# Performance work log

Hardware: AMD Instinct MI355X
Metric: run time of the kernel (lower is better)

Reference implementation:

```python
import jax, jax.numpy as jnp
import numpy as np

K_CLUSTERS = 64   # hardcoded k=64 in get_kmenas_prototypes
KM_ITERS = 10     # KMeans(max_iter=10)


def _kmeans_one_hot(x):
    """x: (B, N, C) points. Returns one-hot cluster masks (B, K, N)."""
    B, N, C = x.shape
    init_idx = jnp.round(jnp.linspace(0, N - 1, K_CLUSTERS)).astype(jnp.int32)

    def per_item(pts):  # (N, C)
        p2 = (pts * pts).sum(-1)  # (N,)

        def assign(cent):
            c2 = (cent * cent).sum(-1)
            d = p2[:, None] + c2[None, :] - 2.0 * (pts @ cent.T)  # (N, K)
            return jnp.argmin(d, axis=1)

        def step(i, cent):
            lab = assign(cent)
            oh = jax.nn.one_hot(lab, K_CLUSTERS, dtype=pts.dtype)  # (N, K)
            cnt = oh.sum(0)
            sums = oh.T @ pts  # (K, C)
            return jnp.where(cnt[:, None] > 0, sums / jnp.maximum(cnt, 1.0)[:, None], cent)

        cent = jax.lax.fori_loop(0, KM_ITERS, step, pts[init_idx])
        lab = assign(cent)
        return jax.nn.one_hot(lab, K_CLUSTERS, dtype=pts.dtype).T  # (K, N)

    return jax.vmap(per_item)(x)


def reference(target, ref, sqz_w, sqz_b, slot_w, slot_b, Wq, Wk, Wv, Wo):
    B, Cin, H, W = target.shape
    Cout = sqz_w.shape[0]
    R = ref.shape[0]
    HW = H * W

    # 1x1 convs
    sqz_target = jnp.einsum('bchw,oc->bohw', target, sqz_w) + sqz_b[None, :, None, None]
    slot_target = jnp.einsum('bchw,oc->bohw', target, slot_w) + slot_b[None, :, None, None]

    xt = sqz_target.reshape(B, Cout, HW)  # (B, C, HW)

    # KMeans prototypes (clustering mask is detached in the original)
    mask = jax.lax.stop_gradient(_kmeans_one_hot(xt.transpose(0, 2, 1)))  # (B, K, HW)
    target_pt = jnp.einsum('bkn,bcn->bkc', mask, xt)  # (B, K, C)

    # slot prototypes: softmax over slot/channel dim (dim=1)
    ss = jax.nn.softmax(slot_target.reshape(B, -1, HW), axis=1)  # (B, S, HW)
    slot_pt = jnp.einsum('bsn,bcn->bsc', ss, xt)  # (B, S, C)
    slot_mask = ss.reshape(B, -1, H, W)

    # ref prototypes: mask = feature itself, softmax over spatial dim (dim=2)
    sqz_ref = jnp.einsum('rbchw,oc->rbohw', ref, sqz_w) + sqz_b[None, None, :, None, None]
    xr = sqz_ref.reshape(R, B, Cout, HW)
    ssr = jax.nn.softmax(xr, axis=3)
    ref_pt = jnp.einsum('rbcn,rbdn->rbcd', ssr, xr)  # (R, B, C, C)

    # Feature_Aggregation_Transformer: cross-attention, queries = kmeans tokens,
    # kv = flattened ref prototype tokens (b, R*C, C)
    kv = ref_pt.transpose(1, 0, 2, 3).reshape(B, R * Cout, Cout)
    q = target_pt @ Wq
    k = kv @ Wk
    v = kv @ Wv
    scale = 1.0 / jnp.sqrt(jnp.asarray(Cout, q.dtype))
    attn = jax.nn.softmax(jnp.einsum('bqc,bkc->bqk', q, k) * scale, axis=-1)
    agg_pt = jnp.einsum('bqk,bkc->bqc', attn, v) @ Wo + target_pt  # (B, K, C)

    return (sqz_target, agg_pt, ref_pt, slot_pt, slot_mask)


def setup_inputs() -> dict:
    key = jax.random.key(0)
    ks = jax.random.split(key, 12)
    B, Cin, Cout, S, H, W, R = 8, 512, 128, 16, 64, 64, 3
    w = lambda k, shp: (jax.random.normal(k, shp, dtype=jnp.float32) * 0.02)
    return {
        'target': jax.random.normal(ks[0], (B, Cin, H, W), dtype=jnp.float32),
        'ref': jax.random.normal(ks[1], (R, B, Cin, H, W), dtype=jnp.float32),
        'sqz_w': w(ks[2], (Cout, Cin)),
        'sqz_b': jnp.zeros((Cout,), dtype=jnp.float32),
        'slot_w': w(ks[3], (S, Cin)),
        'slot_b': jnp.zeros((S,), dtype=jnp.float32),
        'Wq': w(ks[4], (Cout, Cout)),
        'Wk': w(ks[5], (Cout, Cout)),
        'Wv': w(ks[6], (Cout, Cout)),
        'Wo': w(ks[7], (Cout, Cout)),
    }
```

## Files before the change

kernel.cpp:

```cpp
#include <hip/hip_runtime.h>

#define NB 8
#define CIN 512
#define CO 128
#define NS 16
#define NHW 4096
#define NR 3
#define NK 64
#define KMITERS 10

typedef __attribute__((ext_vector_type(8))) short s16x8;
typedef __attribute__((ext_vector_type(4))) float f32x4;

static __device__ __forceinline__ void bsplit(float x, short& h, short& l) {
    union { float f; unsigned u; } a; a.f = x;
    h = (short)(a.u >> 16);
    union { unsigned u; float f; } hf; hf.u = a.u & 0xFFFF0000u;
    union { float f; unsigned u; } r; r.f = x - hf.f;
    l = (short)(r.u >> 16);
}

__global__ __launch_bounds__(256) void conv_mfma(const float* __restrict__ X,
    const float* __restrict__ Wt, const float* __restrict__ bias, float* __restrict__ out)
{
    __shared__ short sWh[128 * 40];
    __shared__ short sWl[128 * 40];
    __shared__ float sX[32 * 133];
    const int g = blockIdx.y;
    const int n0 = blockIdx.x * 128;
    const int tid = threadIdx.x;
    const int lane = tid & 63, w = tid >> 6;
    const int l15 = lane & 15, quad = lane >> 4;
    const int wm = (w & 1) * 64, wn = (w >> 1) * 64;

    f32x4 acc[4][4];
#pragma unroll
    for (int i = 0; i < 4; ++i)
#pragma unroll
        for (int j = 0; j < 4; ++j) acc[i][j] = (f32x4){0.f, 0.f, 0.f, 0.f};

    for (int c0 = 0; c0 < CIN; c0 += 32) {
        if (c0) __syncthreads();
#pragma unroll
        for (int r = 0; r < 4; ++r) {
            int e = r * 1024 + tid * 4;
            int m = e >> 5, cc = e & 31;
            const float4 wv = *(const float4*)&Wt[(size_t)m * CIN + c0 + cc];
            short h0, l0, h1, l1, h2, l2, h3, l3;
            bsplit(wv.x, h0, l0); bsplit(wv.y, h1, l1);
            bsplit(wv.z, h2, l2); bsplit(wv.w, h3, l3);
            *(short4*)&sWh[m * 40 + cc] = make_short4(h0, h1, h2, h3);
            *(short4*)&sWl[m * 40 + cc] = make_short4(l0, l1, l2, l3);
        }
#pragma unroll
        for (int r = 0; r < 4; ++r) {
            int e = r * 1024 + tid * 4;
            int k = e >> 7, n = e & 127;
            const float4 xv = *(const float4*)&X[((size_t)g * CIN + c0 + k) * NHW + n0 + n];
            float* p = &sX[k * 133 + n];
            p[0] = xv.x; p[1] = xv.y; p[2] = xv.z; p[3] = xv.w;
        }
        __syncthreads();

        s16x8 ah[4], al[4];
#pragma unroll
        for (int mt = 0; mt < 4; ++mt) {
            int m = wm + mt * 16 + l15;
            ah[mt] = *(const s16x8*)&sWh[m * 40 + quad * 8];
            al[mt] = *(const s16x8*)&sWl[m * 40 + quad * 8];
        }
#pragma unroll
        for (int nt = 0; nt < 4; ++nt) {
            int n = wn + nt * 16 + l15;
            s16x8 bh, bl;
#pragma unroll
            for (int jj = 0; jj < 8; ++jj) {
                float xv = sX[(quad * 8 + jj) * 133 + n];
                short h, l; bsplit(xv, h, l);
                bh[jj] = h; bl[jj] = l;
            }
#pragma unroll
            for (int mt = 0; mt < 4; ++mt) {
                acc[mt][nt] = __builtin_amdgcn_mfma_f32_16x16x32_bf16(ah[mt], bh, acc[mt][nt], 0, 0, 0);
                acc[mt][nt] = __builtin_amdgcn_mfma_f32_16x16x32_bf16(ah[mt], bl, acc[mt][nt], 0, 0, 0);
                acc[mt][nt] = __builtin_amdgcn_mfma_f32_16x16x32_bf16(al[mt], bh, acc[mt][nt], 0, 0, 0);
            }
        }
    }
#pragma unroll
    for (int mt = 0; mt < 4; ++mt) {
#pragma unroll
        for (int reg = 0; reg < 4; ++reg) {
            int m = wm + mt * 16 + quad * 4 + reg;
            float bv = bias[m];
#pragma unroll
            for (int nt = 0; nt < 4; ++nt) {
                int n = wn + nt * 16 + l15;
                out[((size_t)g * CO + m) * NHW + n0 + n] = acc[mt][nt][reg] + bv;
            }
        }
    }
}

template<int BM, int BN, int BK, int TM, int TN>
__global__ __launch_bounds__(256) void conv1x1(const float* __restrict__ X,
    const float* __restrict__ Wt, const float* __restrict__ bias,
    float* __restrict__ outf)
{
    __shared__ float sW[BK][BM + 1];
    __shared__ float sX2[BK][BN + 1];
    const int g  = blockIdx.z;
    const int m0 = blockIdx.y * BM;
    const int n0 = blockIdx.x * BN;
    const int tid = threadIdx.x;
    const int tn = tid % (BN / TN);
    const int tm = tid / (BN / TN);
    const int O = gridDim.y * BM;

    float acc[TM][TN];
#pragma unroll
    for (int i = 0; i < TM; ++i)
#pragma unroll
        for (int j = 0; j < TN; ++j) acc[i][j] = 0.f;

    for (int c0 = 0; c0 < CIN; c0 += BK) {
#pragma unroll
        for (int idx = tid; idx < BM * BK; idx += 256) {
            int k = idx % BK, i = idx / BK;
            sW[k][i] = Wt[(size_t)(m0 + i) * CIN + c0 + k];
        }
#pragma unroll
        for (int idx = tid; idx < BK * BN; idx += 256) {
            int j = idx % BN, k = idx / BN;
            sX2[k][j] = X[((size_t)g * CIN + c0 + k) * NHW + n0 + j];
        }
        __syncthreads();
#pragma unroll
        for (int k = 0; k < BK; ++k) {
            float a[TM], bb[TN];
#pragma unroll
            for (int i = 0; i < TM; ++i) a[i] = sW[k][tm * TM + i];
#pragma unroll
            for (int j = 0; j < TN; ++j) bb[j] = sX2[k][tn * TN + j];
#pragma unroll
            for (int i = 0; i < TM; ++i)
#pragma unroll
                for (int j = 0; j < TN; ++j) acc[i][j] = fmaf(a[i], bb[j], acc[i][j]);
        }
        __syncthreads();
    }
#pragma unroll
    for (int i = 0; i < TM; ++i) {
        int m = m0 + tm * TM + i;
        float bv = bias[m];
#pragma unroll
        for (int j = 0; j < TN; ++j) {
            int n = n0 + tn * TN + j;
            outf[((size_t)g * O + m) * NHW + n] = acc[i][j] + bv;
        }
    }
}

__global__ void km_init(const float* __restrict__ xt, float* __restrict__ cent) {
    int idx = blockIdx.x * 256 + threadIdx.x;
    if (idx >= NB * NK * CO) return;
    int c = idx % CO;
    int k = (idx / CO) % NK;
    int b = idx / (CO * NK);
    cent[idx] = xt[((size_t)b * CO + c) * NHW + 65 * k];
}

__global__ __launch_bounds__(256) void km_label(const float* __restrict__ xt,
    const float* __restrict__ cent, float* __restrict__ psums, float* __restrict__ pcnt)
{
    __shared__ float sCent[64 * 129];
    __shared__ float sXs[32 * 133];
    __shared__ float sC2[64];
    __shared__ float sCnt[64];
    __shared__ int sLab[128];
    const int b = blockIdx.y, nb = blockIdx.x;
    const int n0 = nb * 128;
    const int tid = threadIdx.x;

#pragma unroll
    for (int r = 0; r < 8; ++r) {
        int e = r * 1024 + tid * 4;
        int k = e >> 7, c = e & 127;
        const float4 cv = *(const float4*)&cent[((size_t)b * NK + k) * CO + c];
        float* p = &sCent[k * 129 + c];
        p[0] = cv.x; p[1] = cv.y; p[2] = cv.z; p[3] = cv.w;
    }
    __syncthreads();
    if (tid < 64) {
        float s = 0.f;
        for (int c = 0; c < CO; ++c) { float v = sCent[tid * 129 + c]; s = fmaf(v, v, s); }
        sC2[tid] = s;
    }

    const int tn = tid & 7, tm = tid >> 3;
    float dot[4][8];
    float p2[4];
#pragma unroll
    for (int i = 0; i < 4; ++i) {
        p2[i] = 0.f;
#pragma unroll
        for (int j = 0; j < 8; ++j) dot[i][j] = 0.f;
    }
    for (int cc = 0; cc < 4; ++cc) {
        __syncthreads();
#pragma unroll
        for (int r = 0; r < 4; ++r) {
            int e = r * 1024 + tid * 4;
            int c = e >> 7, n = e & 127;
            const float4 xv = *(const float4*)&xt[((size_t)b * CO + cc * 32 + c) * NHW + n0 + n];
            float* p = &sXs[c * 133 + n];
            p[0] = xv.x; p[1] = xv.y; p[2] = xv.z; p[3] = xv.w;
        }
        __syncthreads();
        for (int c4 = 0; c4 < 8; ++c4) {
            float xv[4][4];
#pragma unroll
            for (int j = 0; j < 4; ++j)
#pragma unroll
                for (int i = 0; i < 4; ++i)
                    xv[j][i] = sXs[(c4 * 4 + j) * 133 + tm * 4 + i];
#pragma unroll
            for (int j = 0; j < 4; ++j)
#pragma unroll
                for (int i = 0; i < 4; ++i)
                    p2[i] = fmaf(xv[j][i], xv[j][i], p2[i]);
#pragma unroll
            for (int jj = 0; jj < 8; ++jj) {
                int k = tn * 8 + jj;
#pragma unroll
                for (int j = 0; j < 4; ++j) {
                    float cv = sCent[k * 129 + cc * 32 + c4 * 4 + j];
#pragma unroll
                    for (int i = 0; i < 4; ++i)
                        dot[i][jj] = fmaf(xv[j][i], cv, dot[i][jj]);
                }
            }
        }
    }
#pragma unroll
    for (int i = 0; i < 4; ++i) {
        int lab = tn * 8;
        float bd = p2[i] + sC2[tn * 8] - 2.f * dot[i][0];
#pragma unroll
        for (int jj = 1; jj < 8; ++jj) {
            int k = tn * 8 + jj;
            float d = p2[i] + sC2[k] - 2.f * dot[i][jj];
            if (d < bd) { bd = d; lab = k; }
        }
#pragma unroll
        for (int off = 1; off < 8; off <<= 1) {
            float d2 = __shfl_xor(bd, off);
            int l2 = __shfl_xor(lab, off);
            if (d2 < bd || (d2 == bd && l2 < lab)) { bd = d2; lab = l2; }
        }
        if (tn == 0) sLab[tm * 4 + i] = lab;
    }
    __syncthreads();
    for (int e = tid; e < 64 * 129; e += 256) sCent[e] = 0.f;
    if (tid < 64) sCnt[tid] = 0.f;
    __syncthreads();
    if (tid < 128) atomicAdd(&sCnt[sLab[tid]], 1.f);
    const int cq = tid & 31, sh = tid >> 5;
    for (int cc = 0; cc < 4; ++cc) {
        __syncthreads();
#pragma unroll
        for (int r = 0; r < 4; ++r) {
            int e = r * 1024 + tid * 4;
            int c = e >> 7, n = e & 127;
            const float4 xv = *(const float4*)&xt[((size_t)b * CO + cc * 32 + c) * NHW + n0 + n];
            float* p = &sXs[c * 133 + n];
            p[0] = xv.x; p[1] = xv.y; p[2] = xv.z; p[3] = xv.w;
        }
        __syncthreads();
        int c = cc * 32 + cq;
        for (int ii = 0; ii < 16; ++ii) {
            int p = sh * 16 + ii;
            atomicAdd(&sCent[sLab[p] * 129 + c], sXs[cq * 133 + p]);
        }
    }
    __syncthreads();
    float* ps = &psums[((size_t)b * 32 + nb) * (NK * CO)];
    for (int e = tid; e < NK * CO; e += 256) {
        int k = e >> 7, c = e & 127;
        ps[e] = sCent[k * 129 + c];
    }
    if (tid < 64) pcnt[((size_t)b * 32 + nb) * 64 + tid] = sCnt[tid];
}

__global__ void km_update2(float* __restrict__ cent, float* __restrict__ tpt,
    const float* __restrict__ psums, const float* __restrict__ pcnt, int mode)
{
    const int k = blockIdx.x, b = blockIdx.y, c = threadIdx.x;
    float s = 0.f;
    for (int nb = 0; nb < 32; ++nb)
        s += psums[((size_t)b * 32 + nb) * (NK * CO) + k * CO + c];
    if (mode) { tpt[((size_t)b * NK + k) * CO + c] = s; return; }
    float cn = 0.f;
    for (int nb = 0; nb < 32; ++nb)
        cn += pcnt[((size_t)b * 32 + nb) * 64 + k];
    if (cn > 0.f) cent[((size_t)b * NK + k) * CO + c] = s / fmaxf(cn, 1.f);
}

__global__ void slot_softmax(const float* __restrict__ ssb, float* __restrict__ out4) {
    int idx = blockIdx.x * 256 + threadIdx.x;
    if (idx >= NB * NHW) return;
    int b = idx / NHW, n = idx % NHW;
    float v[NS];
    float m = -1e30f;
#pragma unroll
    for (int s = 0; s < NS; ++s) { v[s] = ssb[((size_t)b * NS + s) * NHW + n]; m = fmaxf(m, v[s]); }
    float sum = 0.f;
#pragma unroll
    for (int s = 0; s < NS; ++s) { v[s] = expf(v[s] - m); sum += v[s]; }
    float inv = 1.f / sum;
#pragma unroll
    for (int s = 0; s < NS; ++s)
        out4[((size_t)b * NS + s) * NHW + n] = v[s] * inv;
}

__global__ __launch_bounds__(256) void slot_pt_kernel(const float* __restrict__ ss,
    const float* __restrict__ xt, float* __restrict__ spt)
{
    __shared__ float sS[NS][257];
    __shared__ float sX2[32][257];
    const int b = blockIdx.y;
    const int n0 = blockIdx.x * 256;
    const int tid = threadIdx.x;
    for (int i = tid; i < NS * 256; i += 256) {
        int s = i >> 8, nn = i & 255;
        sS[s][nn] = ss[((size_t)b * NS + s) * NHW + n0 + nn];
    }
    const int c = tid & 31;
    const int sA = tid >> 5;
    for (int cg = 0; cg < 4; ++cg) {
        __syncthreads();
        for (int i = tid; i < 32 * 256; i += 256) {
            int cc = i >> 8, nn = i & 255;
            sX2[cc][nn] = xt[((size_t)b * CO + cg * 32 + cc) * NHW + n0 + nn];
        }
        __syncthreads();
        float a0 = 0.f, a1 = 0.f;
        for (int nn = 0; nn < 256; ++nn) {
            float x = sX2[c][nn];
            a0 = fmaf(x, sS[sA][nn], a0);
            a1 = fmaf(x, sS[sA + 8][nn], a1);
        }
        atomicAdd(&spt[((size_t)b * NS + sA) * CO + cg * 32 + c], a0);
        atomicAdd(&spt[((size_t)b * NS + sA + 8) * CO + cg * 32 + c], a1);
    }
}

__global__ __launch_bounds__(256) void rowstats(const float* __restrict__ xr,
    float* __restrict__ rmax, float* __restrict__ rinv)
{
    const int row = blockIdx.x;
    const float* p = xr + (size_t)row * NHW;
    const int tid = threadIdx.x;
    float v[16];
    float m = -1e30f;
#pragma unroll
    for (int i = 0; i < 16; ++i) { v[i] = p[tid + (i << 8)]; m = fmaxf(m, v[i]); }
#pragma unroll
    for (int off = 32; off; off >>= 1) m = fmaxf(m, __shfl_down(m, off));
    __shared__ float sm[4];
    __shared__ float ss2[4];
    const int wid = tid >> 6, lane = tid & 63;
    if (lane == 0) sm[wid] = m;
    __syncthreads();
    m = fmaxf(fmaxf(sm[0], sm[1]), fmaxf(sm[2], sm[3]));
    float s = 0.f;
#pragma unroll
    for (int i = 0; i < 16; ++i) s += expf(v[i] - m);
#pragma unroll
    for (int off = 32; off; off >>= 1) s += __shfl_down(s, off);
    if (lane == 0) ss2[wid] = s;
    __syncthreads();
    if (tid == 0) {
        rmax[row] = m;
        rinv[row] = 1.f / (ss2[0] + ss2[1] + ss2[2] + ss2[3]);
    }
}

__global__ __launch_bounds__(256) void refpt_mfma(const float* __restrict__ xr,
    const float* __restrict__ rmax, const float* __restrict__ rinv,
    float* __restrict__ refpt)
{
    __shared__ short sSh[128 * 40];
    __shared__ short sSl[128 * 40];
    __shared__ short sXh[128 * 40];
    __shared__ short sXl[128 * 40];
    __shared__ float sMax[CO];
    __shared__ float sInv[CO];
    const int g = blockIdx.y;
    const int n0 = blockIdx.x * 256;
    const int tid = threadIdx.x;
    const int lane = tid & 63, w = tid >> 6;
    const int l15 = lane & 15, quad = lane >> 4;
    const int wm = (w & 1) * 64, wn = (w >> 1) * 64;
    const float* base = xr + (size_t)g * CO * NHW;

    if (tid < CO) {
        sMax[tid] = rmax[g * CO + tid];
        sInv[tid] = rinv[g * CO + tid];
    }

    f32x4 acc[4][4];
#pragma unroll
    for (int i = 0; i < 4; ++i)
#pragma unroll
        for (int j = 0; j < 4; ++j) acc[i][j] = (f32x4){0.f, 0.f, 0.f, 0.f};

    for (int ks = 0; ks < 8; ++ks) {
        __syncthreads();
#pragma unroll
        for (int r = 0; r < 4; ++r) {
            int e = r * 1024 + tid * 4;
            int row = e >> 5, col = e & 31;
            const float4 xv = *(const float4*)&base[(size_t)row * NHW + n0 + ks * 32 + col];
            const float mx = sMax[row], iv = sInv[row];
            short h0, l0, h1, l1, h2, l2, h3, l3;
            bsplit(xv.x, h0, l0); bsplit(xv.y, h1, l1);
            bsplit(xv.z, h2, l2); bsplit(xv.w, h3, l3);
            *(short4*)&sXh[row * 40 + col] = make_short4(h0, h1, h2, h3);
            *(short4*)&sXl[row * 40 + col] = make_short4(l0, l1, l2, l3);
            float s0 = expf(xv.x - mx) * iv, s1 = expf(xv.y - mx) * iv;
            float s2 = expf(xv.z - mx) * iv, s3 = expf(xv.w - mx) * iv;
            bsplit(s0, h0, l0); bsplit(s1, h1, l1);
            bsplit(s2, h2, l2); bsplit(s3, h3, l3);
            *(short4*)&sSh[row * 40 + col] = make_short4(h0, h1, h2, h3);
            *(short4*)&sSl[row * 40 + col] = make_short4(l0, l1, l2, l3);
        }
        __syncthreads();

        s16x8 ah[4], al[4];
#pragma unroll
        for (int mt = 0; mt < 4; ++mt) {
            int m = wm + mt * 16 + l15;
            ah[mt] = *(const s16x8*)&sSh[m * 40 + quad * 8];
            al[mt] = *(const s16x8*)&sSl[m * 40 + quad * 8];
        }
#pragma unroll
        for (int nt = 0; nt < 4; ++nt) {
            int d = wn + nt * 16 + l15;
            s16x8 bh = *(const s16x8*)&sXh[d * 40 + quad * 8];
            s16x8 bl = *(const s16x8*)&sXl[d * 40 + quad * 8];
#pragma unroll
            for (int mt = 0; mt < 4; ++mt) {
                acc[mt][nt] = __builtin_amdgcn_mfma_f32_16x16x32_bf16(ah[mt], bh, acc[mt][nt], 0, 0, 0);
                acc[mt][nt] = __builtin_amdgcn_mfma_f32_16x16x32_bf16(ah[mt], bl, acc[mt][nt], 0, 0, 0);
                acc[mt][nt] = __builtin_amdgcn_mfma_f32_16x16x32_bf16(al[mt], bh, acc[mt][nt], 0, 0, 0);
            }
        }
    }
#pragma unroll
    for (int mt = 0; mt < 4; ++mt) {
#pragma unroll
        for (int reg = 0; reg < 4; ++reg) {
            int m = wm + mt * 16 + quad * 4 + reg;
#pragma unroll
            for (int nt = 0; nt < 4; ++nt) {
                int d = wn + nt * 16 + l15;
                atomicAdd(&refpt[((size_t)g * CO + m) * CO + d], acc[mt][nt][reg]);
            }
        }
    }
}

__global__ void build_kv(const float* __restrict__ refpt, float* __restrict__ kv) {
    int idx = blockIdx.x * 256 + threadIdx.x;
    if (idx >= NB * NR * CO * CO) return;
    int d = idx % CO;
    int j = (idx / CO) % (NR * CO);
    int b = idx / (CO * NR * CO);
    int r = j / CO, cc = j % CO;
    kv[idx] = refpt[(((size_t)r * NB + b) * CO + cc) * CO + d];
}

__global__ void gemm_aw(const float* __restrict__ A, const float* __restrict__ Wm,
                        float* __restrict__ Cm, int M)
{
    int idx = blockIdx.x * 256 + threadIdx.x;
    if (idx >= NB * M * CO) return;
    int c = idx % CO;
    int m = (idx / CO) % M;
    int b = idx / (CO * M);
    const float* ar = A + ((size_t)b * M + m) * CO;
    float acc = 0.f;
    for (int e = 0; e < CO; ++e) acc = fmaf(ar[e], Wm[e * CO + c], acc);
    Cm[idx] = acc;
}

__global__ __launch_bounds__(256) void attn_kernel(const float* __restrict__ qb,
    const float* __restrict__ kb, const float* __restrict__ vb, float* __restrict__ ctx)
{
    __shared__ float sq[CO];
    __shared__ float sl[NR * CO];
    __shared__ float red[4], red2[4];
    const int b = blockIdx.y, i = blockIdx.x;
    const int tid = threadIdx.x;
    if (tid < CO) sq[tid] = qb[((size_t)b * NK + i) * CO + tid];
    __syncthreads();
    const float scale = 0.08838834764831843f;
    for (int j = tid; j < NR * CO; j += 256) {
        const float* kr = kb + ((size_t)b * NR * CO + j) * CO;
        float d = 0.f;
        for (int e = 0; e < CO; ++e) d = fmaf(sq[e], kr[e], d);
        sl[j] = d * scale;
    }
    __syncthreads();
    float m = -1e30f;
    for (int j = tid; j < NR * CO; j += 256) m = fmaxf(m, sl[j]);
#pragma unroll
    for (int off = 32; off; off >>= 1) m = fmaxf(m, __shfl_down(m, off));
    if ((tid & 63) == 0) red[tid >> 6] = m;
    __syncthreads();
    m = fmaxf(fmaxf(red[0], red[1]), fmaxf(red[2], red[3]));
    float s = 0.f;
    for (int j = tid; j < NR * CO; j += 256) { float e = expf(sl[j] - m); sl[j] = e; s += e; }
#pragma unroll
    for (int off = 32; off; off >>= 1) s += __shfl_down(s, off);
    if ((tid & 63) == 0) red2[tid >> 6] = s;
    __syncthreads();
    const float inv = 1.f / (red2[0] + red2[1] + red2[2] + red2[3]);
    if (tid < CO) {
        float acc = 0.f;
        for (int j = 0; j < NR * CO; ++j)
            acc = fmaf(sl[j], vb[((size_t)b * NR * CO + j) * CO + tid], acc);
        ctx[((size_t)b * NK + i) * CO + tid] = acc * inv;
    }
}

__global__ void final_agg(const float* __restrict__ ctx, const float* __restrict__ Wo,
                          const float* __restrict__ tpt, float* __restrict__ out1)
{
    int idx = blockIdx.x * 256 + threadIdx.x;
    if (idx >= NB * NK * CO) return;
    int c = idx % CO;
    const float* cr = ctx + (size_t)(idx / CO) * CO;
    float acc = tpt[idx];
    for (int e = 0; e < CO; ++e) acc = fmaf(cr[e], Wo[e * CO + c], acc);
    out1[idx] = acc;
}

extern "C" void kernel_launch(void* const* d_in, const int* in_sizes, int n_in,
                              void* d_out, int out_size, void* d_ws, size_t ws_size,
                              hipStream_t stream) {
    (void)in_sizes; (void)n_in; (void)out_size; (void)ws_size;
    const float* target = (const float*)d_in[0];
    const float* ref    = (const float*)d_in[1];
    const float* sqz_w  = (const float*)d_in[2];
    const float* sqz_b  = (const float*)d_in[3];
    const float* slot_w = (const float*)d_in[4];
    const float* slot_b = (const float*)d_in[5];
    const float* Wq     = (const float*)d_in[6];
    const float* Wk     = (const float*)d_in[7];
    const float* Wv     = (const float*)d_in[8];
    const float* Wo     = (const float*)d_in[9];

    float* out  = (float*)d_out;
    float* out0 = out;
    float* out1 = out + 4194304;
    float* out2 = out + 4259840;
    float* out3 = out + 4653056;
    float* out4 = out + 4669440;

    float* ws    = (float*)d_ws;
    float* ssb   = ws;
    float* xr    = ssb + 524288;
    float* rmax  = xr + 12582912;
    float* rinv  = rmax + 3072;
    float* cent  = rinv + 3072;
    float* psums = cent + 65536;
    float* pcnt  = psums + 2097152;
    float* tpt   = pcnt + 16384;
    float* kvb   = tpt + 65536;
    float* qb    = kvb + 393216;
    float* kb    = qb + 65536;
    float* vb    = kb + 393216;
    float* ctxb  = vb + 393216;

    hipMemsetAsync(out3, 0, (size_t)16384 * 4, stream);
    hipMemsetAsync(out2, 0, (size_t)393216 * 4, stream);

    conv1x1<64, 64, 32, 4, 4><<<dim3(NHW / 64, CO / 64, NB), 256, 0, stream>>>(
        target, sqz_w, sqz_b, out0);
    conv1x1<16, 64, 32, 1, 4><<<dim3(NHW / 64, 1, NB), 256, 0, stream>>>(
        target, slot_w, slot_b, ssb);
    conv_mfma<<<dim3(NHW / 128, NR * NB), 256, 0, stream>>>(ref, sqz_w, sqz_b, xr);

    km_init<<<(NB * NK * CO + 255) / 256, 256, 0, stream>>>(out0, cent);
    for (int it = 0; it < KMITERS; ++it) {
        km_label<<<dim3(32, NB), 256, 0, stream>>>(out0, cent, psums, pcnt);
        km_update2<<<dim3(NK, NB), 128, 0, stream>>>(cent, tpt, psums, pcnt, 0);
    }
    km_label<<<dim3(32, NB), 256, 0, stream>>>(out0, cent, psums, pcnt);
    km_update2<<<dim3(NK, NB), 128, 0, stream>>>(cent, tpt, psums, pcnt, 1);

    slot_softmax<<<(NB * NHW + 255) / 256, 256, 0, stream>>>(ssb, out4);
    slot_pt_kernel<<<dim3(NHW / 256, NB), 256, 0, stream>>>(out4, out0, out3);

    rowstats<<<NR * NB * CO, 256, 0, stream>>>(xr, rmax, rinv);
    refpt_mfma<<<dim3(NHW / 256, NR * NB), 256, 0, stream>>>(xr, rmax, rinv, out2);

    build_kv<<<(NB * NR * CO * CO + 255) / 256, 256, 0, stream>>>(out2, kvb);
    gemm_aw<<<(NB * NK * CO + 255) / 256, 256, 0, stream>>>(tpt, Wq, qb, NK);
    gemm_aw<<<(NB * NR * CO * CO + 255) / 256, 256, 0, stream>>>(kvb, Wk, kb, NR * CO);
    gemm_aw<<<(NB * NR * CO * CO + 255) / 256, 256, 0, stream>>>(kvb, Wv, vb, NR * CO);
    attn_kernel<<<dim3(NK, NB), 256, 0, stream>>>(qb, kb, vb, ctxb);
    final_agg<<<(NB * NK * CO + 255) / 256, 256, 0, stream>>>(ctxb, Wo, tpt, out1);
}
```

Measured before the change: 1.277 ms.

## Vectorize conv1x1 tiles and widen km_label to 1024 threads

conv1x1 now uses float4 global loads, float4 shared-memory reads and float4 stores, with larger N tiles (128 and 256) and one sync removed per K step. km_label switches to 1024 threads per block with one point per thread group. It stages the whole 128x128 point tile in shared memory once instead of reloading it per channel chunk for both the distance and accumulation phases. The intent is to raise the parallelism of the serial k-means chain (256 blocks only) and cut redundant global reloads, at the cost of much larger shared memory per block (about 100KB) and lower per-thread register reuse.

```diff
diff --git a/kernel.cpp b/kernel.cpp
--- a/kernel.cpp
+++ b/kernel.cpp
@@ -107,15 +107,19 @@
     const float* __restrict__ Wt, const float* __restrict__ bias,
     float* __restrict__ outf)
 {
-    __shared__ float sW[BK][BM + 1];
-    __shared__ float sX2[BK][BN + 1];
+    static_assert(TM == 4 && (TN == 4 || TN == 8), "mapping assumes TM=4");
+    __shared__ float sW[BK][BM + 4];
+    __shared__ float sX2[BK][BN + 4];
     const int g  = blockIdx.z;
     const int m0 = blockIdx.y * BM;
     const int n0 = blockIdx.x * BN;
     const int tid = threadIdx.x;
-    const int tn = tid % (BN / TN);
-    const int tm = tid / (BN / TN);
+    constexpr int NTH_N = BN / TN;
+    const int tn = tid % NTH_N;
+    const int tm = tid / NTH_N;
     const int O = gridDim.y * BM;
+    const int cb0 = tn * 4;
+    const int cb1 = BN / 2 + tn * 4;
 
     float acc[TM][TN];
 #pragma unroll
@@ -124,39 +128,47 @@
         for (int j = 0; j < TN; ++j) acc[i][j] = 0.f;
 
     for (int c0 = 0; c0 < CIN; c0 += BK) {
-#pragma unroll
-        for (int idx = tid; idx < BM * BK; idx += 256) {
-            int k = idx % BK, i = idx / BK;
-            sW[k][i] = Wt[(size_t)(m0 + i) * CIN + c0 + k];
-        }
-#pragma unroll
-        for (int idx = tid; idx < BK * BN; idx += 256) {
-            int j = idx % BN, k = idx / BN;
-            sX2[k][j] = X[((size_t)g * CIN + c0 + k) * NHW + n0 + j];
+        if (c0) __syncthreads();
+        constexpr int F4R = BK / 4;
+        for (int idx4 = tid; idx4 < BM * F4R; idx4 += 256) {
+            int m = idx4 / F4R, cw = (idx4 % F4R) * 4;
+            const float4 wv = *(const float4*)&Wt[(size_t)(m0 + m) * CIN + c0 + cw];
+            sW[cw][m] = wv.x; sW[cw + 1][m] = wv.y;
+            sW[cw + 2][m] = wv.z; sW[cw + 3][m] = wv.w;
+        }
+        constexpr int F4N = BN / 4;
+        for (int idx4 = tid; idx4 < BK * F4N; idx4 += 256) {
+            int k = idx4 / F4N, n4 = (idx4 % F4N) * 4;
+            *(float4*)&sX2[k][n4] =
+                *(const float4*)&X[((size_t)g * CIN + c0 + k) * NHW + n0 + n4];
         }
         __syncthreads();
 #pragma unroll
         for (int k = 0; k < BK; ++k) {
             float a[TM], bb[TN];
-#pragma unroll
-            for (int i = 0; i < TM; ++i) a[i] = sW[k][tm * TM + i];
-#pragma unroll
-            for (int j = 0; j < TN; ++j) bb[j] = sX2[k][tn * TN + j];
+            *(float4*)&a[0] = *(const float4*)&sW[k][tm * 4];
+            *(float4*)&bb[0] = *(const float4*)&sX2[k][cb0];
+            if constexpr (TN == 8)
+                *(float4*)&bb[4] = *(const float4*)&sX2[k][cb1];
 #pragma unroll
             for (int i = 0; i < TM; ++i)
 #pragma unroll
                 for (int j = 0; j < TN; ++j) acc[i][j] = fmaf(a[i], bb[j], acc[i][j]);
         }
-        __syncthreads();
     }
 #pragma unroll
     for (int i = 0; i < TM; ++i) {
-        int m = m0 + tm * TM + i;
+        int m = m0 + tm * 4 + i;
         float bv = bias[m];
-#pragma unroll
-        for (int j = 0; j < TN; ++j) {
-            int n = n0 + tn * TN + j;
-            outf[((size_t)g * O + m) * NHW + n] = acc[i][j] + bv;
+        float4 o0;
+        o0.x = acc[i][0] + bv; o0.y = acc[i][1] + bv;
+        o0.z = acc[i][2] + bv; o0.w = acc[i][3] + bv;
+        *(float4*)&outf[((size_t)g * O + m) * NHW + n0 + cb0] = o0;
+        if constexpr (TN == 8) {
+            float4 o1;
+            o1.x = acc[i][4] + bv; o1.y = acc[i][5] + bv;
+            o1.z = acc[i][6] + bv; o1.w = acc[i][7] + bv;
+            *(float4*)&outf[((size_t)g * O + m) * NHW + n0 + cb1] = o1;
         }
     }
 }
@@ -170,11 +182,11 @@
     cent[idx] = xt[((size_t)b * CO + c) * NHW + 65 * k];
 }
 
-__global__ __launch_bounds__(256) void km_label(const float* __restrict__ xt,
+__global__ __launch_bounds__(1024) void km_label(const float* __restrict__ xt,
     const float* __restrict__ cent, float* __restrict__ psums, float* __restrict__ pcnt)
 {
     __shared__ float sCent[64 * 129];
-    __shared__ float sXs[32 * 133];
+    __shared__ float sXs[128 * 133];
     __shared__ float sC2[64];
     __shared__ float sCnt[64];
     __shared__ int sLab[128];
@@ -183,73 +195,61 @@
     const int tid = threadIdx.x;
 
 #pragma unroll
-    for (int r = 0; r < 8; ++r) {
-        int e = r * 1024 + tid * 4;
+    for (int r = 0; r < 2; ++r) {
+        int e = r * 4096 + tid * 4;
         int k = e >> 7, c = e & 127;
         const float4 cv = *(const float4*)&cent[((size_t)b * NK + k) * CO + c];
         float* p = &sCent[k * 129 + c];
         p[0] = cv.x; p[1] = cv.y; p[2] = cv.z; p[3] = cv.w;
     }
+#pragma unroll
+    for (int r = 0; r < 4; ++r) {
+        int e = r * 4096 + tid * 4;
+        int c = e >> 7, n = e & 127;
+        const float4 xv = *(const float4*)&xt[((size_t)b * CO + c) * NHW + n0 + n];
+        float* p = &sXs[c * 133 + n];
+        p[0] = xv.x; p[1] = xv.y; p[2] = xv.z; p[3] = xv.w;
+    }
     __syncthreads();
     if (tid < 64) {
         float s = 0.f;
         for (int c = 0; c < CO; ++c) { float v = sCent[tid * 129 + c]; s = fmaf(v, v, s); }
         sC2[tid] = s;
     }
+    __syncthreads();
 
     const int tn = tid & 7, tm = tid >> 3;
-    float dot[4][8];
-    float p2[4];
-#pragma unroll
-    for (int i = 0; i < 4; ++i) {
-        p2[i] = 0.f;
-#pragma unroll
-        for (int j = 0; j < 8; ++j) dot[i][j] = 0.f;
-    }
+    float dot[8];
+    float p2 = 0.f;
+#pragma unroll
+    for (int j = 0; j < 8; ++j) dot[j] = 0.f;
     for (int cc = 0; cc < 4; ++cc) {
-        __syncthreads();
-#pragma unroll
-        for (int r = 0; r < 4; ++r) {
-            int e = r * 1024 + tid * 4;
-            int c = e >> 7, n = e & 127;
-            const float4 xv = *(const float4*)&xt[((size_t)b * CO + cc * 32 + c) * NHW + n0 + n];
-            float* p = &sXs[c * 133 + n];
-            p[0] = xv.x; p[1] = xv.y; p[2] = xv.z; p[3] = xv.w;
-        }
-        __syncthreads();
         for (int c4 = 0; c4 < 8; ++c4) {
-            float xv[4][4];
+            float xv[4];
 #pragma unroll
             for (int j = 0; j < 4; ++j)
-#pragma unroll
-                for (int i = 0; i < 4; ++i)
-                    xv[j][i] = sXs[(c4 * 4 + j) * 133 + tm * 4 + i];
+                xv[j] = sXs[(cc * 32 + c4 * 4 + j) * 133 + tm];
 #pragma unroll
             for (int j = 0; j < 4; ++j)
-#pragma unroll
-                for (int i = 0; i < 4; ++i)
-                    p2[i] = fmaf(xv[j][i], xv[j][i], p2[i]);
+                p2 = fmaf(xv[j], xv[j], p2);
 #pragma unroll
             for (int jj = 0; jj < 8; ++jj) {
                 int k = tn * 8 + jj;
 #pragma unroll
                 for (int j = 0; j < 4; ++j) {
                     float cv = sCent[k * 129 + cc * 32 + c4 * 4 + j];
-#pragma unroll
-                    for (int i = 0; i < 4; ++i)
-                        dot[i][jj] = fmaf(xv[j][i], cv, dot[i][jj]);
+                    dot[jj] = fmaf(xv[j], cv, dot[jj]);
                 }
             }
         }
     }
-#pragma unroll
-    for (int i = 0; i < 4; ++i) {
+    {
         int lab = tn * 8;
-        float bd = p2[i] + sC2[tn * 8] - 2.f * dot[i][0];
+        float bd = p2 + sC2[tn * 8] - 2.f * dot[0];
 #pragma unroll
         for (int jj = 1; jj < 8; ++jj) {
             int k = tn * 8 + jj;
-            float d = p2[i] + sC2[k] - 2.f * dot[i][jj];
+            float d = p2 + sC2[k] - 2.f * dot[jj];
             if (d < bd) { bd = d; lab = k; }
         }
 #pragma unroll
@@ -258,34 +258,26 @@
             int l2 = __shfl_xor(lab, off);
             if (d2 < bd || (d2 == bd && l2 < lab)) { bd = d2; lab = l2; }
         }
-        if (tn == 0) sLab[tm * 4 + i] = lab;
-    }
-    __syncthreads();
-    for (int e = tid; e < 64 * 129; e += 256) sCent[e] = 0.f;
+        if (tn == 0) sLab[tm] = lab;
+    }
+    __syncthreads();
+    for (int e = tid; e < 64 * 129; e += 1024) sCent[e] = 0.f;
     if (tid < 64) sCnt[tid] = 0.f;
     __syncthreads();
     if (tid < 128) atomicAdd(&sCnt[sLab[tid]], 1.f);
-    const int cq = tid & 31, sh = tid >> 5;
-    for (int cc = 0; cc < 4; ++cc) {
-        __syncthreads();
-#pragma unroll
-        for (int r = 0; r < 4; ++r) {
-            int e = r * 1024 + tid * 4;
-            int c = e >> 7, n = e & 127;
-            const float4 xv = *(const float4*)&xt[((size_t)b * CO + cc * 32 + c) * NHW + n0 + n];
-            float* p = &sXs[c * 133 + n];
-            p[0] = xv.x; p[1] = xv.y; p[2] = xv.z; p[3] = xv.w;
-        }
-        __syncthreads();
-        int c = cc * 32 + cq;
-        for (int ii = 0; ii < 16; ++ii) {
-            int p = sh * 16 + ii;
-            atomicAdd(&sCent[sLab[p] * 129 + c], sXs[cq * 133 + p]);
+    if (tid < 256) {
+        const int cq = tid & 31, sh = tid >> 5;
+        for (int cc = 0; cc < 4; ++cc) {
+            int c = cc * 32 + cq;
+            for (int ii = 0; ii < 16; ++ii) {
+                int p = sh * 16 + ii;
+                atomicAdd(&sCent[sLab[p] * 129 + c], sXs[c * 133 + p]);
+            }
         }
     }
     __syncthreads();
     float* ps = &psums[((size_t)b * 32 + nb) * (NK * CO)];
-    for (int e = tid; e < NK * CO; e += 256) {
+    for (int e = tid; e < NK * CO; e += 1024) {
         int k = e >> 7, c = e & 127;
         ps[e] = sCent[k * 129 + c];
     }
@@ -587,18 +579,18 @@
     hipMemsetAsync(out3, 0, (size_t)16384 * 4, stream);
     hipMemsetAsync(out2, 0, (size_t)393216 * 4, stream);
 
-    conv1x1<64, 64, 32, 4, 4><<<dim3(NHW / 64, CO / 64, NB), 256, 0, stream>>>(
+    conv1x1<64, 128, 32, 4, 8><<<dim3(NHW / 128, CO / 64, NB), 256, 0, stream>>>(
         target, sqz_w, sqz_b, out0);
-    conv1x1<16, 64, 32, 1, 4><<<dim3(NHW / 64, 1, NB), 256, 0, stream>>>(
+    conv1x1<16, 256, 32, 4, 4><<<dim3(NHW / 256, 1, NB), 256, 0, stream>>>(
         target, slot_w, slot_b, ssb);
     conv_mfma<<<dim3(NHW / 128, NR * NB), 256, 0, stream>>>(ref, sqz_w, sqz_b, xr);
 
     km_init<<<(NB * NK * CO + 255) / 256, 256, 0, stream>>>(out0, cent);
     for (int it = 0; it < KMITERS; ++it) {
-        km_label<<<dim3(32, NB), 256, 0, stream>>>(out0, cent, psums, pcnt);
+        km_label<<<dim3(32, NB), 1024, 0, stream>>>(out0, cent, psums, pcnt);
         km_update2<<<dim3(NK, NB), 128, 0, stream>>>(cent, tpt, psums, pcnt, 0);
     }
-    km_label<<<dim3(32, NB), 256, 0, stream>>>(out0, cent, psums, pcnt);
+    km_label<<<dim3(32, NB), 1024, 0, stream>>>(out0, cent, psums, pcnt);
     km_update2<<<dim3(NK, NB), 128, 0, stream>>>(cent, tpt, psums, pcnt, 1);
 
     slot_softmax<<<(NB * NHW + 255) / 256, 256, 0, stream>>>(ssb, out4);
```

Result: slower. 1.323 ms (+3.6%).
